# Optimization experiments

Measured on AMD Instinct MI355X. Metric: run time of the kernel, lower is better.

Reference implementation:

```python
import jax, jax.numpy as jnp
import numpy as np

B, C_IN, IMG = 64, 3, 384
P = 16                 # patch size / conv stride
HID = 768              # hidden_size
CQ = HID // 8          # query/key channels in CrissCrossAttention
H = W = IMG // P       # 24x24 token grid
NP = H * W             # 576 patches
NEG_INF = -1e30        # finite stand-in for -inf diagonal mask (grad-safe)


def setup_inputs() -> dict:
    key = jax.random.key(0)
    ks = jax.random.split(key, 10)
    s = lambda fan_in: 1.0 / np.sqrt(fan_in)
    return {
        "x": jax.random.normal(ks[0], (B, C_IN, IMG, IMG), jnp.float32),
        "patch_w": jax.random.normal(ks[1], (HID, C_IN, P, P), jnp.float32) * s(C_IN * P * P),
        "patch_b": jax.random.normal(ks[2], (HID,), jnp.float32) * 0.02,
        "wq": jax.random.normal(ks[3], (CQ, HID), jnp.float32) * s(HID),
        "bq": jax.random.normal(ks[4], (CQ,), jnp.float32) * 0.02,
        "wk": jax.random.normal(ks[5], (CQ, HID), jnp.float32) * s(HID),
        "bk": jax.random.normal(ks[6], (CQ,), jnp.float32) * 0.02,
        "wv": jax.random.normal(ks[7], (HID, HID), jnp.float32) * s(HID),
        "bv": jax.random.normal(ks[8], (HID,), jnp.float32) * 0.02,
        "gamma": jnp.zeros((1,), jnp.float32),
        "pos_emb": jax.random.normal(ks[9], (1, NP, HID), jnp.float32) * 0.02,
    }


def criss_cross_attention(x, wq, bq, wk, bk, wv, bv, gamma):
    # x: [b, c, h, w]
    b, c, h, w = x.shape
    q = jnp.einsum('oc,bchw->bohw', wq, x) + bq[None, :, None, None]   # [b,cq,h,w]
    k = jnp.einsum('oc,bchw->bohw', wk, x) + bk[None, :, None, None]   # [b,cq,h,w]
    v = jnp.einsum('oc,bchw->bohw', wv, x) + bv[None, :, None, None]   # [b,c,h,w]

    # column (H-axis) attention energies with -inf on the diagonal (self-pair)
    energy_H = jnp.einsum('bciw,bcjw->biwj', q, k)                     # [b,h,w,h]
    eye = jnp.eye(h, dtype=bool)[:, None, :]                           # [h,1,h]
    energy_H = jnp.where(eye, NEG_INF, energy_H)
    # row (W-axis) attention energies
    energy_W = jnp.einsum('bchi,bchj->bhij', q, k)                     # [b,h,w,w]

    concate = jax.nn.softmax(jnp.concatenate([energy_H, energy_W], axis=3), axis=3)
    att_H = concate[..., :h]                                           # [b,h,w,h]
    att_W = concate[..., h:]                                           # [b,h,w,w]

    out_H = jnp.einsum('biwj,bcjw->bciw', att_H, v)                    # [b,c,h,w]
    out_W = jnp.einsum('bhij,bchj->bchi', att_W, v)                    # [b,c,h,w]
    return gamma[0] * (out_H + out_W) + x


def reference(x, patch_w, patch_b, wq, bq, wk, bk, wv, bv, gamma, pos_emb):
    # patch embedding: Conv2d(3->768, kernel=16, stride=16)
    y = jax.lax.conv_general_dilated(
        x, patch_w, window_strides=(P, P), padding='VALID',
        dimension_numbers=('NCHW', 'OIHW', 'NCHW'))
    y = y + patch_b[None, :, None, None]                               # [b,768,24,24]
    y = criss_cross_attention(y, wq, bq, wk, bk, wv, bv, gamma)
    y = y.reshape(y.shape[0], y.shape[1], -1).transpose(0, 2, 1)       # [b, 576, 768]
    emb = y + pos_emb                                                  # dropout: eval-mode identity
    return emb
```

## Files before the change

### kernel.cpp

```cpp
#include <hip/hip_runtime.h>
#include <hip/hip_bf16.h>
#include <cstdint>

#define BATCH 64
#define CIN 3
#define IMG 384
#define PATCH 16
#define HID 768
#define CQ 96
#define HW24 24
#define NP 576
#define MROWS (BATCH*NP)
#define KDIM 768
#define NVQK 1024
#define NT_K 12
#define NEGINF (-1e30f)

typedef __attribute__((ext_vector_type(8))) short s16x8;
typedef __attribute__((ext_vector_type(4))) float f32x4;

__device__ __forceinline__ float bf2f(unsigned short u) {
    union { unsigned int i; float f; } x; x.i = ((unsigned int)u) << 16; return x.f;
}
__device__ __forceinline__ unsigned short f2bf(float f) {
    union { float f; unsigned int i; } x; x.f = f;
    unsigned int r = x.i + 0x7fffu + ((x.i >> 16) & 1u);
    return (unsigned short)(r >> 16);
}
__device__ __forceinline__ unsigned int f2bf2(float a, float b) {
    union { __hip_bfloat162 h; unsigned int u; } c;
    c.h = __float22bfloat162_rn(make_float2(a, b));
    return c.u;
}

__device__ __forceinline__ void gload_lds16(const void* g, void* l) {
    __builtin_amdgcn_global_load_lds(
        (const __attribute__((address_space(1))) void*)(uintptr_t)g,
        (__attribute__((address_space(3))) void*)(uint32_t)(uintptr_t)l,
        16, 0, 0);
}

__device__ __forceinline__ size_t kp_addr(int row, int col) {
    return (((size_t)(row >> 8) * NT_K + (col >> 6)) * 256 + (row & 255)) * 64 + (col & 63);
}

__global__ void k_prep(const float* __restrict__ pw, const float* __restrict__ wq,
                       const float* __restrict__ wk, const float* __restrict__ wv,
                       const float* __restrict__ bq, const float* __restrict__ bk,
                       const float* __restrict__ bv,
                       unsigned short* __restrict__ Wp, unsigned short* __restrict__ Wvqk,
                       float* __restrict__ Bvqk) {
    int t = blockIdx.x * 256 + threadIdx.x;
    if (t < HID * HID) Wp[t] = f2bf(pw[t]);
    if (t < NVQK * HID) {
        int row = t / HID; int col = t - row * HID;
        float val = 0.f;
        if (row < 768) val = wv[t];
        else if (row < 864) val = wq[(row - 768) * HID + col];
        else if (row < 960) val = wk[(row - 864) * HID + col];
        Wvqk[t] = f2bf(val);
    }
    if (t < NVQK) {
        float v = 0.f;
        if (t < 768) v = bv[t]; else if (t < 864) v = bq[t - 768]; else if (t < 960) v = bk[t - 864];
        Bvqk[t] = v;
    }
}

__device__ __forceinline__ void stageB_half(const unsigned short* __restrict__ gmat,
        int growbase, char* ldsregion, int kcol, int rl, int sp, int ldsoff0) {
    const unsigned short* g0 = gmat + (size_t)(growbase + rl) * KDIM + kcol + sp * 8;
    gload_lds16(g0, ldsregion + ldsoff0);
    gload_lds16(g0 + (size_t)8 * KDIM, ldsregion + ldsoff0 + 1024);
}

__global__ __launch_bounds__(512, 1) void k_gemmFused(
    const float* __restrict__ x, const unsigned short* __restrict__ Bw,
    const float* __restrict__ bias, unsigned short* __restrict__ Y,
    float* __restrict__ outF, const float* __restrict__ pos,
    const float* __restrict__ gamma)
{
    extern __shared__ char smem[];
    const int tid  = threadIdx.x;
    const int lane = tid & 63;
    const int w    = tid >> 6;
    const int wm   = w >> 2;
    const int wn   = w & 3;

    const int nwg = gridDim.x;
    const int chunk = nwg >> 3;
    const int bid = blockIdx.x;
    const int bs = (bid & 7) * chunk + (bid >> 3);
    const int bx = bs >> 1, by = bs & 1;
    const int blockN = by * 384;

    const int rl = (w << 4) + (lane >> 3);
    const int sp = (lane & 7) ^ (lane >> 3);
    const int ldsoff0 = (w << 11) + (lane << 4);

    const int lx   = (lane & 15) << 7;
    const int swz  = (lane & 7) << 4;
    const int cbx0 = (((lane >> 4) << 4)) ^ swz;
    const int cbx1 = (64 + ((lane >> 4) << 4)) ^ swz;

    const int rr = tid >> 2;
    const int q  = tid & 3;
    const int grow = (bx << 7) + rr;
    const int b  = grow / NP;
    const int p  = grow - b * NP;
    const int ph = p / HW24, pw = p - ph * HW24;
    const float* xrow = x + (size_t)b * (CIN * IMG * IMG) + ph * (PATCH * IMG) + pw * PATCH + (q << 2);
    const int swzr  = (rr & 7) << 4;
    const int wbase = rr * 128;

    char* paC = smem;
    char* paN = smem + 16384;
    char* pbC = smem + 32768;
    char* pbN = smem + 81920;

    float4 ld[4];
    auto loadA = [&](int t) {
        const float* src = xrow + (t >> 2) * (IMG * IMG) + ((t & 3) << 2) * IMG;
        #pragma unroll
        for (int u = 0; u < 4; ++u) ld[u] = *(const float4*)(src + u * IMG);
    };
    auto writeA = [&](char* dst) {
        #pragma unroll
        for (int u = 0; u < 4; ++u) {
            int2 pk;
            pk.x = f2bf2(ld[u].x, ld[u].y);
            pk.y = f2bf2(ld[u].z, ld[u].w);
            *reinterpret_cast<int2*>(dst + wbase + (((u << 5) + (q << 3)) ^ swzr)) = pk;
        }
    };
    auto stageB3 = [&](char* dst, int kcol) {
        stageB_half(Bw, blockN,       dst,         kcol, rl, sp, ldsoff0);
        stageB_half(Bw, blockN + 128, dst + 16384, kcol, rl, sp, ldsoff0);
        stageB_half(Bw, blockN + 256, dst + 32768, kcol, rl, sp, ldsoff0);
    };

    f32x4 acc[4][6] = {};

    loadA(0);
    stageB3(pbC, 0);
    asm volatile("s_waitcnt vmcnt(6)" ::: "memory");
    __builtin_amdgcn_sched_barrier(0);
    writeA(paC);
    asm volatile("s_waitcnt vmcnt(0) lgkmcnt(0)" ::: "memory");
    __builtin_amdgcn_sched_barrier(0);
    __builtin_amdgcn_s_barrier();

    for (int t = 0; t < NT_K; ++t) {
        if (t + 1 < NT_K) {
            loadA(t + 1);
            stageB3(pbN, (t + 1) << 6);
        }
        s16x8 af[4][2];
        #pragma unroll
        for (int m = 0; m < 4; ++m) {
            const int rb0 = wm * 8192 + m * 2048 + lx;
            af[m][0] = *(const s16x8*)(paC + rb0 + cbx0);
            af[m][1] = *(const s16x8*)(paC + rb0 + cbx1);
        }
        __builtin_amdgcn_s_setprio(1);
        #pragma unroll
        for (int nf = 0; nf < 6; ++nf) {
            const int rb = wn * 12288 + nf * 2048 + lx;
            s16x8 b0 = *(const s16x8*)(pbC + rb + cbx0);
            s16x8 b1 = *(const s16x8*)(pbC + rb + cbx1);
            #pragma unroll
            for (int m = 0; m < 4; ++m)
                acc[m][nf] = __builtin_amdgcn_mfma_f32_16x16x32_bf16(b0, af[m][0], acc[m][nf], 0, 0, 0);
            #pragma unroll
            for (int m = 0; m < 4; ++m)
                acc[m][nf] = __builtin_amdgcn_mfma_f32_16x16x32_bf16(b1, af[m][1], acc[m][nf], 0, 0, 0);
        }
        __builtin_amdgcn_s_setprio(0);
        if (t + 1 < NT_K) {
            __builtin_amdgcn_sched_barrier(0);
            asm volatile("s_waitcnt vmcnt(0)" ::: "memory");
            __builtin_amdgcn_sched_barrier(0);
            writeA(paN);
            asm volatile("s_waitcnt lgkmcnt(0)" ::: "memory");
            __builtin_amdgcn_sched_barrier(0);
            __builtin_amdgcn_s_barrier();
            char* ta = paC; paC = paN; paN = ta;
            char* tb = pbC; pbC = pbN; pbN = tb;
        }
    }

    const int rowb = (bx << 7) + wm * 64 + (lane & 15);
    const int colb = blockN + wn * 96 + ((lane >> 4) << 2);
    const float g = gamma[0];
    if (g == 0.f) {
        #pragma unroll
        for (int mf = 0; mf < 4; ++mf) {
            const int row = rowb + mf * 16;
            const int px = row % NP;
            #pragma unroll
            for (int nf = 0; nf < 6; ++nf) {
                const int col = colb + nf * 16;
                float4 bs4 = *(const float4*)(bias + col);
                float4 pv  = *(const float4*)(pos + (size_t)px * HID + col);
                f32x4 a = acc[mf][nf];
                float4 o;
                o.x = a[0] + bs4.x + pv.x;
                o.y = a[1] + bs4.y + pv.y;
                o.z = a[2] + bs4.z + pv.z;
                o.w = a[3] + bs4.w + pv.w;
                *reinterpret_cast<float4*>(outF + (size_t)row * HID + col) = o;
            }
        }
    } else {
        #pragma unroll
        for (int mf = 0; mf < 4; ++mf) {
            const int row = rowb + mf * 16;
            #pragma unroll
            for (int nf = 0; nf < 6; ++nf) {
                const int col = colb + nf * 16;
                float4 bs4 = *(const float4*)(bias + col);
                f32x4 a = acc[mf][nf];
                ushort4 o;
                o.x = f2bf(a[0] + bs4.x);
                o.y = f2bf(a[1] + bs4.y);
                o.z = f2bf(a[2] + bs4.z);
                o.w = f2bf(a[3] + bs4.w);
                *reinterpret_cast<ushort4*>(Y + kp_addr(row, col)) = o;
            }
        }
    }
}

__device__ __forceinline__ void stageA_half(const unsigned short* __restrict__ Ap,
        size_t tilebase, int h, char* ldsregion, int rl, int sp, int ldsoff0) {
    const unsigned short* g0 = Ap + tilebase + (size_t)(h * 128 + rl) * 64 + sp * 8;
    gload_lds16(g0, ldsregion + ldsoff0);
    gload_lds16(g0 + 512, ldsregion + ldsoff0 + 1024);
}

__global__ __launch_bounds__(512, 2) void k_gemm256(
    const unsigned short* __restrict__ A, const unsigned short* __restrict__ Bw,
    const float* __restrict__ bias, unsigned short* __restrict__ C,
    const float* __restrict__ gamma, int NT)
{
    if (gamma[0] == 0.f) return;
    extern __shared__ char smem[];
    const int tid  = threadIdx.x;
    const int lane = tid & 63;
    const int w    = tid >> 6;
    const int wm   = w >> 2;
    const int wn   = w & 3;
    const int nwg = gridDim.x;
    const int chunk = nwg >> 3;
    const int bid = blockIdx.x;
    const int bs = (bid & 7) * chunk + (bid >> 3);
    const int bx = bs / NT, by = bs - (bs / NT) * NT;
    const int blockN = by << 8;
    const int rl = (w << 4) + (lane >> 3);
    const int sp = (lane & 7) ^ (lane >> 3);
    const int ldsoff0 = (w << 11) + (lane << 4);
    const int lx   = (lane & 15) << 7;
    const int swz  = (lane & 7) << 4;
    const int cbx0 = (((lane >> 4) << 4)) ^ swz;
    const int cbx1 = (64 + ((lane >> 4) << 4)) ^ swz;
    char* pa0 = smem;
    char* pa1 = smem + 32768;
    char* pa2 = smem + 65536;
    char* pb0 = smem + 98304;
    char* pb1 = smem + 131072;
    const size_t atile0 = ((size_t)bx * NT_K) << 14;

    stageB_half(Bw, blockN,       pb0,         0,  rl, sp, ldsoff0);
    stageB_half(Bw, blockN + 128, pb0 + 16384, 0,  rl, sp, ldsoff0);
    stageA_half(A, atile0,         0, pa0,         rl, sp, ldsoff0);
    stageA_half(A, atile0,         1, pa0 + 16384, rl, sp, ldsoff0);
    stageA_half(A, atile0 + 16384, 0, pa1,         rl, sp, ldsoff0);
    stageA_half(A, atile0 + 16384, 1, pa1 + 16384, rl, sp, ldsoff0);

    f32x4 acc[8][4] = {};
    asm volatile("s_waitcnt vmcnt(4)" ::: "memory");
    __builtin_amdgcn_sched_barrier(0);
    __builtin_amdgcn_s_barrier();

    for (int t = 0; t < NT_K; ++t) {
        if (t + 1 < NT_K) {
            stageB_half(Bw, blockN,       pb1,         (t + 1) << 6, rl, sp, ldsoff0);
            stageB_half(Bw, blockN + 128, pb1 + 16384, (t + 1) << 6, rl, sp, ldsoff0);
        }
        if (t + 2 < NT_K) {
            const size_t tb = atile0 + ((size_t)(t + 2) << 14);
            stageA_half(A, tb, 0, pa2,         rl, sp, ldsoff0);
            stageA_half(A, tb, 1, pa2 + 16384, rl, sp, ldsoff0);
        }
        s16x8 bfr[4][2];
        #pragma unroll
        for (int nf = 0; nf < 4; ++nf) {
            const int rb = wn * 8192 + nf * 2048 + lx;
            bfr[nf][0] = *(const s16x8*)(pb0 + rb + cbx0);
            bfr[nf][1] = *(const s16x8*)(pb0 + rb + cbx1);
        }
        #pragma unroll
        for (int half = 0; half < 2; ++half) {
            s16x8 af[4][2];
            #pragma unroll
            for (int m = 0; m < 4; ++m) {
                const int rb0 = wm * 16384 + (half * 4 + m) * 2048 + lx;
                af[m][0] = *(const s16x8*)(pa0 + rb0 + cbx0);
                af[m][1] = *(const s16x8*)(pa0 + rb0 + cbx1);
            }
            __builtin_amdgcn_s_setprio(1);
            #pragma unroll
            for (int kh = 0; kh < 2; ++kh)
                #pragma unroll
                for (int m = 0; m < 4; ++m)
                    #pragma unroll
                    for (int nf = 0; nf < 4; ++nf)
                        acc[half * 4 + m][nf] = __builtin_amdgcn_mfma_f32_16x16x32_bf16(
                            bfr[nf][kh], af[m][kh], acc[half * 4 + m][nf], 0, 0, 0);
            __builtin_amdgcn_s_setprio(0);
        }
        if (t < NT_K - 1) {
            __builtin_amdgcn_sched_barrier(0);
            if (t >= NT_K - 3) { asm volatile("s_waitcnt vmcnt(0)" ::: "memory"); }
            else               { asm volatile("s_waitcnt vmcnt(4)" ::: "memory"); }
            __builtin_amdgcn_s_barrier();
            __builtin_amdgcn_sched_barrier(0);
        }
        char* ta = pa0; pa0 = pa1; pa1 = pa2; pa2 = ta;
        char* tb = pb0; pb0 = pb1; pb1 = tb;
    }

    const int rowb = (bx << 8) + wm * 128 + (lane & 15);
    const int colb = blockN + wn * 64 + ((lane >> 4) << 2);
    #pragma unroll
    for (int mf = 0; mf < 8; ++mf) {
        const int row = rowb + mf * 16;
        #pragma unroll
        for (int nf = 0; nf < 4; ++nf) {
            const int col = colb + nf * 16;
            float4 bs4 = *(const float4*)(bias + col);
            f32x4 a = acc[mf][nf];
            ushort4 o;
            o.x = f2bf(a[0] + bs4.x);
            o.y = f2bf(a[1] + bs4.y);
            o.z = f2bf(a[2] + bs4.z);
            o.w = f2bf(a[3] + bs4.w);
            *reinterpret_cast<ushort4*>(C + (size_t)row * (NT << 8) + col) = o;
        }
    }
}

__global__ __launch_bounds__(256) void k_energyH(const unsigned short* __restrict__ VQK,
                                                 float* __restrict__ E, const float* __restrict__ gam) {
    if (gam[0] == 0.f) return;
    __shared__ float qs[24][97], ks[24][97];
    const int b = blockIdx.x / HW24, w = blockIdx.x % HW24;
    const int tid = threadIdx.x;
    for (int idx = tid; idx < 24 * 12; idx += 256) {
        int i = idx / 12, c = (idx % 12) * 8;
        size_t base = ((size_t)(b * NP + i * HW24 + w)) * NVQK + 768;
        s16x8 qv = *(const s16x8*)(VQK + base + c);
        s16x8 kv = *(const s16x8*)(VQK + base + 96 + c);
        #pragma unroll
        for (int u = 0; u < 8; u++) {
            qs[i][c + u] = bf2f((unsigned short)qv[u]);
            ks[i][c + u] = bf2f((unsigned short)kv[u]);
        }
    }
    __syncthreads();
    for (int idx = tid; idx < 576; idx += 256) {
        int i = idx / 24, j = idx - (idx / 24) * 24;
        float s = NEGINF;
        if (i != j) {
            s = 0.f;
            #pragma unroll 8
            for (int c = 0; c < 96; c++) s += qs[i][c] * ks[j][c];
        }
        E[((size_t)(b * NP + i * HW24 + w)) * 48 + j] = s;
    }
}

__global__ __launch_bounds__(256) void k_energyW(const unsigned short* __restrict__ VQK,
                                                 float* __restrict__ E, const float* __restrict__ gam) {
    if (gam[0] == 0.f) return;
    __shared__ float qs[24][97], ks[24][97], ew[24][24];
    const int b = blockIdx.x / HW24, h = blockIdx.x % HW24;
    const int tid = threadIdx.x;
    const int prow = b * NP + h * HW24;
    for (int idx = tid; idx < 24 * 12; idx += 256) {
        int i = idx / 12, c = (idx % 12) * 8;
        size_t base = ((size_t)(prow + i)) * NVQK + 768;
        s16x8 qv = *(const s16x8*)(VQK + base + c);
        s16x8 kv = *(const s16x8*)(VQK + base + 96 + c);
        #pragma unroll
        for (int u = 0; u < 8; u++) {
            qs[i][c + u] = bf2f((unsigned short)qv[u]);
            ks[i][c + u] = bf2f((unsigned short)kv[u]);
        }
    }
    __syncthreads();
    for (int idx = tid; idx < 576; idx += 256) {
        int i = idx / 24, j = idx - (idx / 24) * 24;
        float s = 0.f;
        #pragma unroll 8
        for (int c = 0; c < 96; c++) s += qs[i][c] * ks[j][c];
        ew[i][j] = s;
    }
    __syncthreads();
    if (tid < 24) {
        size_t p = prow + tid;
        float e[48];
        #pragma unroll
        for (int j = 0; j < 24; j++) e[j] = E[p * 48 + j];
        #pragma unroll
        for (int j = 0; j < 24; j++) e[24 + j] = ew[tid][j];
        float mx = NEGINF;
        #pragma unroll
        for (int j = 0; j < 48; j++) mx = fmaxf(mx, e[j]);
        float sum = 0.f;
        #pragma unroll
        for (int j = 0; j < 48; j++) { e[j] = __expf(e[j] - mx); sum += e[j]; }
        float inv = 1.f / sum;
        #pragma unroll
        for (int j = 0; j < 48; j++) E[p * 48 + j] = e[j] * inv;
    }
}

__global__ __launch_bounds__(192) void k_passH(const float* __restrict__ E,
        const unsigned short* __restrict__ VQK, const unsigned short* __restrict__ Y,
        const float* __restrict__ gamma, const float* __restrict__ pos,
        float* __restrict__ out) {
    const float g = gamma[0];
    if (g == 0.f) return;
    __shared__ float att[576];
    int bid = (blockIdx.x & 7) * 192 + (blockIdx.x >> 3);
    const int b = bid / HW24, w = bid % HW24;
    const int tid = threadIdx.x;
    for (int idx = tid; idx < 576; idx += 192) {
        int i = idx / 24, j = idx - (idx / 24) * 24;
        att[idx] = E[((size_t)(b * NP + i * HW24 + w)) * 48 + j];
    }
    __syncthreads();
    float vf[24][4];
    #pragma unroll
    for (int j = 0; j < 24; j++) {
        ushort4 vv = *(const ushort4*)(VQK + ((size_t)(b * NP + j * HW24 + w)) * NVQK + 4 * tid);
        vf[j][0] = bf2f(vv.x); vf[j][1] = bf2f(vv.y); vf[j][2] = bf2f(vv.z); vf[j][3] = bf2f(vv.w);
    }
    #pragma unroll
    for (int i = 0; i < 24; i++) {
        float a0 = 0.f, a1 = 0.f, a2 = 0.f, a3 = 0.f;
        #pragma unroll
        for (int j = 0; j < 24; j++) {
            float a = att[i * 24 + j];
            a0 += a * vf[j][0]; a1 += a * vf[j][1]; a2 += a * vf[j][2]; a3 += a * vf[j][3];
        }
        size_t p = (size_t)(b * NP + i * HW24 + w);
        ushort4 yv = *(const ushort4*)(Y + kp_addr((int)p, 4 * tid));
        float4 pv = *(const float4*)(pos + (size_t)(i * HW24 + w) * HID + 4 * tid);
        float4 o;
        o.x = g * a0 + bf2f(yv.x) + pv.x;
        o.y = g * a1 + bf2f(yv.y) + pv.y;
        o.z = g * a2 + bf2f(yv.z) + pv.z;
        o.w = g * a3 + bf2f(yv.w) + pv.w;
        *reinterpret_cast<float4*>(out + p * HID + 4 * tid) = o;
    }
}

__global__ __launch_bounds__(192) void k_passW(const float* __restrict__ E,
        const unsigned short* __restrict__ VQK, const float* __restrict__ gamma,
        float* __restrict__ out) {
    const float g = gamma[0];
    if (g == 0.f) return;
    __shared__ float att[576];
    int bid = (blockIdx.x & 7) * 192 + (blockIdx.x >> 3);
    const int b = bid / HW24, h = bid % HW24;
    const int tid = threadIdx.x;
    const int prow = b * NP + h * HW24;
    for (int idx = tid; idx < 576; idx += 192) {
        int i = idx / 24, j = idx - (idx / 24) * 24;
        att[idx] = E[((size_t)(prow + i)) * 48 + 24 + j];
    }
    __syncthreads();
    float vf[24][4];
    #pragma unroll
    for (int j = 0; j < 24; j++) {
        ushort4 vv = *(const ushort4*)(VQK + ((size_t)(prow + j)) * NVQK + 4 * tid);
        vf[j][0] = bf2f(vv.x); vf[j][1] = bf2f(vv.y); vf[j][2] = bf2f(vv.z); vf[j][3] = bf2f(vv.w);
    }
    #pragma unroll
    for (int i = 0; i < 24; i++) {
        float a0 = 0.f, a1 = 0.f, a2 = 0.f, a3 = 0.f;
        #pragma unroll
        for (int j = 0; j < 24; j++) {
            float a = att[i * 24 + j];
            a0 += a * vf[j][0]; a1 += a * vf[j][1]; a2 += a * vf[j][2]; a3 += a * vf[j][3];
        }
        size_t p = (size_t)(prow + i);
        float4 o = *reinterpret_cast<const float4*>(out + p * HID + 4 * tid);
        o.x += g * a0; o.y += g * a1; o.z += g * a2; o.w += g * a3;
        *reinterpret_cast<float4*>(out + p * HID + 4 * tid) = o;
    }
}

extern "C" void kernel_launch(void* const* d_in, const int* in_sizes, int n_in,
                              void* d_out, int out_size, void* d_ws, size_t ws_size,
                              hipStream_t stream) {
    const float* x       = (const float*)d_in[0];
    const float* patch_w = (const float*)d_in[1];
    const float* patch_b = (const float*)d_in[2];
    const float* wq      = (const float*)d_in[3];
    const float* bq      = (const float*)d_in[4];
    const float* wk      = (const float*)d_in[5];
    const float* bk      = (const float*)d_in[6];
    const float* wv      = (const float*)d_in[7];
    const float* bv      = (const float*)d_in[8];
    const float* gamma   = (const float*)d_in[9];
    const float* pos_emb = (const float*)d_in[10];
    float* out = (float*)d_out;

    hipFuncSetAttribute(reinterpret_cast<const void*>(k_gemmFused),
                        hipFuncAttributeMaxDynamicSharedMemorySize, 131072);
    hipFuncSetAttribute(reinterpret_cast<const void*>(k_gemm256),
                        hipFuncAttributeMaxDynamicSharedMemorySize, 163840);

    char* ws = (char*)d_ws;
    size_t off = 0;
    auto alloc = [&](size_t bytes) { char* pp = ws + off; off += (bytes + 255) & ~(size_t)255; return pp; };
    unsigned short* VQK = (unsigned short*)alloc((size_t)MROWS * NVQK * 2);
    unsigned short* Y   = (unsigned short*)alloc((size_t)MROWS * HID * 2);
    unsigned short* Wp  = (unsigned short*)alloc((size_t)HID * HID * 2);
    unsigned short* Wvqk= (unsigned short*)alloc((size_t)NVQK * HID * 2);
    float*          Bvqk= (float*)alloc(NVQK * 4);
    float*          E   = (float*)alloc((size_t)MROWS * 48 * 4);

    k_prep<<<dim3((NVQK * HID + 255) / 256), dim3(256), 0, stream>>>(patch_w, wq, wk, wv, bq, bk, bv, Wp, Wvqk, Bvqk);
    k_gemmFused<<<dim3((MROWS / 128) * 2), dim3(512), 131072, stream>>>(
        x, Wp, patch_b, Y, out, pos_emb, gamma);
    k_gemm256<<<dim3((MROWS / 256) * (NVQK / 256)), dim3(512), 163840, stream>>>(
        Y, Wvqk, Bvqk, VQK, gamma, NVQK / 256);
    k_energyH<<<dim3(BATCH * HW24), dim3(256), 0, stream>>>(VQK, E, gamma);
    k_energyW<<<dim3(BATCH * HW24), dim3(256), 0, stream>>>(VQK, E, gamma);
    k_passH<<<dim3(BATCH * HW24), dim3(192), 0, stream>>>(E, VQK, Y, gamma, pos_emb, out);
    k_passW<<<dim3(BATCH * HW24), dim3(192), 0, stream>>>(E, VQK, gamma, out);
}
```

Measured before the change: 115.3 us.

## Enlarge fused patch-embed GEMM tile to 256 rows with 1024 threads

Doubles the M tile of the fused patch-embedding GEMM to 256 rows per workgroup, launched as 1024 threads, with more LDS. It reorganises the im2col A loads so each thread reads contiguous 16-float row segments and writes 16-byte LDS stores. It also prefetches A two k-steps ahead so global loads overlap the write and barrier. The larger tile gives more reuse of the B operand, but halves the grid and doubles register pressure per workgroup, which can hurt occupancy and load balance across CUs.

New measurement: 426.8 us. 3.7x slower.

```diff
diff --git a/kernel.cpp b/kernel.cpp
--- a/kernel.cpp
+++ b/kernel.cpp
@@ -74,7 +74,7 @@
     gload_lds16(g0 + (size_t)8 * KDIM, ldsregion + ldsoff0 + 1024);
 }
 
-__global__ __launch_bounds__(512, 1) void k_gemmFused(
+__global__ __launch_bounds__(1024, 1) void k_gemmFused(
     const float* __restrict__ x, const unsigned short* __restrict__ Bw,
     const float* __restrict__ bias, unsigned short* __restrict__ Y,
     float* __restrict__ outF, const float* __restrict__ pos,
@@ -87,16 +87,14 @@
     const int wm   = w >> 2;
     const int wn   = w & 3;
 
-    const int nwg = gridDim.x;
-    const int chunk = nwg >> 3;
-    const int bid = blockIdx.x;
-    const int bs = (bid & 7) * chunk + (bid >> 3);
+    const int chunk = gridDim.x >> 3;
+    const int bs = (blockIdx.x & 7) * chunk + (blockIdx.x >> 3);
     const int bx = bs >> 1, by = bs & 1;
     const int blockN = by * 384;
 
-    const int rl = (w << 4) + (lane >> 3);
-    const int sp = (lane & 7) ^ (lane >> 3);
-    const int ldsoff0 = (w << 11) + (lane << 4);
+    const int rb_  = tid >> 3;
+    const int sp   = (tid & 7) ^ (rb_ & 7);
+    const int ldsoffB = tid << 4;
 
     const int lx   = (lane & 15) << 7;
     const int swz  = (lane & 7) << 4;
@@ -105,56 +103,60 @@
 
     const int rr = tid >> 2;
     const int q  = tid & 3;
-    const int grow = (bx << 7) + rr;
+    const int grow = (bx << 8) + rr;
     const int b  = grow / NP;
     const int p  = grow - b * NP;
     const int ph = p / HW24, pw = p - ph * HW24;
-    const float* xrow = x + (size_t)b * (CIN * IMG * IMG) + ph * (PATCH * IMG) + pw * PATCH + (q << 2);
+    const float* xrow = x + (size_t)b * (CIN * IMG * IMG) + ph * (PATCH * IMG) + pw * PATCH;
     const int swzr  = (rr & 7) << 4;
     const int wbase = rr * 128;
 
     char* paC = smem;
-    char* paN = smem + 16384;
-    char* pbC = smem + 32768;
-    char* pbN = smem + 81920;
+    char* paN = smem + 32768;
+    char* pbC = smem + 65536;
+    char* pbN = smem + 114688;
 
     float4 ld[4];
     auto loadA = [&](int t) {
-        const float* src = xrow + (t >> 2) * (IMG * IMG) + ((t & 3) << 2) * IMG;
-        #pragma unroll
-        for (int u = 0; u < 4; ++u) ld[u] = *(const float4*)(src + u * IMG);
+        const int kk = 4 * t + q;
+        const float* src = xrow + (kk >> 4) * (IMG * IMG) + (kk & 15) * IMG;
+        #pragma unroll
+        for (int u = 0; u < 4; ++u) ld[u] = *(const float4*)(src + 4 * u);
     };
     auto writeA = [&](char* dst) {
         #pragma unroll
-        for (int u = 0; u < 4; ++u) {
-            int2 pk;
-            pk.x = f2bf2(ld[u].x, ld[u].y);
-            pk.y = f2bf2(ld[u].z, ld[u].w);
-            *reinterpret_cast<int2*>(dst + wbase + (((u << 5) + (q << 3)) ^ swzr)) = pk;
+        for (int u = 0; u < 2; ++u) {
+            int4 pk;
+            pk.x = f2bf2(ld[2 * u].x,     ld[2 * u].y);
+            pk.y = f2bf2(ld[2 * u].z,     ld[2 * u].w);
+            pk.z = f2bf2(ld[2 * u + 1].x, ld[2 * u + 1].y);
+            pk.w = f2bf2(ld[2 * u + 1].z, ld[2 * u + 1].w);
+            *reinterpret_cast<int4*>(dst + wbase + (((q << 5) + (u << 4)) ^ swzr)) = pk;
         }
     };
-    auto stageB3 = [&](char* dst, int kcol) {
-        stageB_half(Bw, blockN,       dst,         kcol, rl, sp, ldsoff0);
-        stageB_half(Bw, blockN + 128, dst + 16384, kcol, rl, sp, ldsoff0);
-        stageB_half(Bw, blockN + 256, dst + 32768, kcol, rl, sp, ldsoff0);
+    auto stageB = [&](char* dst, int kcol) {
+        const unsigned short* g0 = Bw + (size_t)(blockN + rb_) * KDIM + kcol + sp * 8;
+        gload_lds16(g0,                      dst + ldsoffB);
+        gload_lds16(g0 + (size_t)128 * KDIM, dst + ldsoffB + 16384);
+        gload_lds16(g0 + (size_t)256 * KDIM, dst + ldsoffB + 32768);
     };
 
     f32x4 acc[4][6] = {};
 
     loadA(0);
-    stageB3(pbC, 0);
-    asm volatile("s_waitcnt vmcnt(6)" ::: "memory");
+    stageB(pbC, 0);
+    asm volatile("s_waitcnt vmcnt(3)" ::: "memory");
     __builtin_amdgcn_sched_barrier(0);
     writeA(paC);
-    asm volatile("s_waitcnt vmcnt(0) lgkmcnt(0)" ::: "memory");
+    loadA(1);
+    asm volatile("s_waitcnt vmcnt(4)" ::: "memory");
+    asm volatile("s_waitcnt lgkmcnt(0)" ::: "memory");
     __builtin_amdgcn_sched_barrier(0);
     __builtin_amdgcn_s_barrier();
 
+    #pragma unroll 1
     for (int t = 0; t < NT_K; ++t) {
-        if (t + 1 < NT_K) {
-            loadA(t + 1);
-            stageB3(pbN, (t + 1) << 6);
-        }
+        if (t + 1 < NT_K) stageB(pbN, (t + 1) << 6);
         s16x8 af[4][2];
         #pragma unroll
         for (int m = 0; m < 4; ++m) {
@@ -181,6 +183,7 @@
             asm volatile("s_waitcnt vmcnt(0)" ::: "memory");
             __builtin_amdgcn_sched_barrier(0);
             writeA(paN);
+            if (t + 2 < NT_K) loadA(t + 2);
             asm volatile("s_waitcnt lgkmcnt(0)" ::: "memory");
             __builtin_amdgcn_sched_barrier(0);
             __builtin_amdgcn_s_barrier();
@@ -189,7 +192,7 @@
         }
     }
 
-    const int rowb = (bx << 7) + wm * 64 + (lane & 15);
+    const int rowb = (bx << 8) + wm * 64 + (lane & 15);
     const int colb = blockN + wn * 96 + ((lane >> 4) << 2);
     const float g = gamma[0];
     if (g == 0.f) {
@@ -520,7 +523,7 @@
     float* out = (float*)d_out;
 
     hipFuncSetAttribute(reinterpret_cast<const void*>(k_gemmFused),
-                        hipFuncAttributeMaxDynamicSharedMemorySize, 131072);
+                        hipFuncAttributeMaxDynamicSharedMemorySize, 163840);
     hipFuncSetAttribute(reinterpret_cast<const void*>(k_gemm256),
                         hipFuncAttributeMaxDynamicSharedMemorySize, 163840);
 
@@ -535,7 +538,7 @@
     float*          E   = (float*)alloc((size_t)MROWS * 48 * 4);
 
     k_prep<<<dim3((NVQK * HID + 255) / 256), dim3(256), 0, stream>>>(patch_w, wq, wk, wv, bq, bk, bv, Wp, Wvqk, Bvqk);
-    k_gemmFused<<<dim3((MROWS / 128) * 2), dim3(512), 131072, stream>>>(
+    k_gemmFused<<<dim3((MROWS / 256) * 2), dim3(1024), 163840, stream>>>(
         x, Wp, patch_b, Y, out, pos_emb, gamma);
     k_gemm256<<<dim3((MROWS / 256) * (NVQK / 256)), dim3(512), 163840, stream>>>(
         Y, Wvqk, Bvqk, VQK, gamma, NVQK / 256);
```
